# Kernel optimization log

Measured on AMD Instinct MI355X. Metric: run time of the kernel, lower is better.

Reference implementation:

```python
import jax, jax.numpy as jnp
import numpy as np

B = 1024
FEAT_C = [64, 64, 128, 256, 512]    # channel dim of each intermediate feature map
SPATIAL = [1024, 1024, 256, 64, 16]  # flattened HxW of each map (32x32 input)
STRIDES = [1, 1, 2, 4, 8]
NUM_CLASS = 10


def _conv(x, w, b, s):
    y = jax.lax.conv_general_dilated(x, w, (s, s), 'SAME',
                                     dimension_numbers=('NCHW', 'OIHW', 'NCHW'))
    return y + b[None, :, None, None]


def setup_inputs() -> dict:
    key = jax.random.key(0)
    ks = iter(jax.random.split(key, 64))
    nrm = lambda shape, scale=1.0: jax.random.normal(next(ks), shape, jnp.float32) * scale
    inp = {'x': nrm((B, 3, 32, 32))}
    inp['noise_w'] = nrm((15, 3, 3, 3), 0.1)
    inp['noise_b'] = nrm((15,), 0.01)
    for i, (c, s) in enumerate(zip(FEAT_C, SPATIAL)):
        inp[f'feat_w{i}'] = nrm((c, 3, 3, 3), 0.2)
        inp[f'feat_b{i}'] = nrm((c,), 0.01)
        inp[f'mu_w{i}'] = nrm((NUM_CLASS, s), 1.0 / np.sqrt(s))
        inp[f'mu_b{i}'] = nrm((NUM_CLASS,), 0.01)
        inp[f'std_w{i}'] = nrm((NUM_CLASS, s), 1.0 / np.sqrt(s))
        inp[f'std_b{i}'] = nrm((NUM_CLASS,), 0.01)
    inp['clf_w'] = nrm((1, 5), 0.5)
    inp['clf_b'] = nrm((1,), 0.01)
    return inp


def _forward(x, noise_w, noise_b, feat_ws, feat_bs, mu_ws, mu_bs, std_ws, std_bs, clf_w, clf_b):
    Bsz = x.shape[0]
    # noised_img = x.repeat([1,5,1,1]) + noise_layer(x)   -> [B,15,32,32]
    noised = jnp.tile(x, (1, 5, 1, 1)) + _conv(x, noise_w, noise_b, 1)
    ekey = jax.random.key(42)
    scores, means, stds = [], [], []
    for i in range(5):
        xi = noised[:, 3 * i:3 * (i + 1)]
        # stand-in for pretrained_model.intermediate_forward -> [B, C_i, S_i]
        f = _conv(xi, feat_ws[i], feat_bs[i], STRIDES[i]).reshape(Bsz, FEAT_C[i], -1)
        # Linear over flattened-spatial dim then transpose(1,2): [B, 10, C_i]
        x_mean = jnp.einsum('bcs,ks->bkc', f, mu_ws[i]) + mu_bs[i][None, :, None]
        x_std = jnp.einsum('bcs,ks->bkc', f, std_ws[i]) + std_bs[i][None, :, None]
        # original builds dense diag(std)^2 [B,10,C,C]; diagonal exploited analytically
        var = x_std * x_std                       # diag entries of x_variance (== scale_tril)
        eps = jax.random.normal(jax.random.fold_in(ekey, i), x_mean.shape, x_mean.dtype)
        d = var * eps                             # sample - mean = scale_tril @ eps (diagonal)
        # -0.5 * d^T inv(diag(var)) d, inverse done analytically instead of torch.inverse
        mahal = -0.5 * jnp.sum(d * d / var, axis=-1)   # [B, 10]
        idx = jnp.argmax(mahal, axis=1)
        scores.append(jnp.max(mahal, axis=1))
        means.append(jnp.take_along_axis(x_mean, idx[:, None, None], axis=1)[:, 0, :])
        stds.append(jnp.take_along_axis(x_std, idx[:, None, None], axis=1)[:, 0, :])
    score_stack = jnp.stack(scores, axis=1)       # [B, 5]
    out = (score_stack @ clf_w.T + clf_b)[:, 0]   # classifier Linear(5,1), squeeze(-1)
    return out, means, stds


def reference(x, noise_w, noise_b,
              feat_w0, feat_b0, mu_w0, mu_b0, std_w0, std_b0,
              feat_w1, feat_b1, mu_w1, mu_b1, std_w1, std_b1,
              feat_w2, feat_b2, mu_w2, mu_b2, std_w2, std_b2,
              feat_w3, feat_b3, mu_w3, mu_b3, std_w3, std_b3,
              feat_w4, feat_b4, mu_w4, mu_b4, std_w4, std_b4,
              clf_w, clf_b):
    feat_ws = [feat_w0, feat_w1, feat_w2, feat_w3, feat_w4]
    feat_bs = [feat_b0, feat_b1, feat_b2, feat_b3, feat_b4]
    mu_ws = [mu_w0, mu_w1, mu_w2, mu_w3, mu_w4]
    mu_bs = [mu_b0, mu_b1, mu_b2, mu_b3, mu_b4]
    std_ws = [std_w0, std_w1, std_w2, std_w3, std_w4]
    std_bs = [std_b0, std_b1, std_b2, std_b3, std_b4]
    out, means, stds = _forward(x, noise_w, noise_b, feat_ws, feat_bs,
                                mu_ws, mu_bs, std_ws, std_bs, clf_w, clf_b)
    return (out, *means, *stds)
```

## Files before the change

### kernel.cpp

```cpp
#include <hip/hip_runtime.h>
#include <cstdint>

#define B_SZ 1024

__host__ __device__ inline void tf2x32(uint32_t k0, uint32_t k1,
                                       uint32_t x0, uint32_t x1,
                                       uint32_t& o0, uint32_t& o1) {
  uint32_t ks2 = 0x1BD11BDAu ^ k0 ^ k1;
#define TF_RND(r) { x0 += x1; x1 = (x1 << (r)) | (x1 >> (32 - (r))); x1 ^= x0; }
  x0 += k0; x1 += k1;
  TF_RND(13) TF_RND(15) TF_RND(26) TF_RND(6)
  x0 += k1; x1 += ks2 + 1u;
  TF_RND(17) TF_RND(29) TF_RND(16) TF_RND(24)
  x0 += ks2; x1 += k0 + 2u;
  TF_RND(13) TF_RND(15) TF_RND(26) TF_RND(6)
  x0 += k0; x1 += k1 + 3u;
  TF_RND(17) TF_RND(29) TF_RND(16) TF_RND(24)
  x0 += k1; x1 += ks2 + 4u;
  TF_RND(13) TF_RND(15) TF_RND(26) TF_RND(6)
  x0 += ks2; x1 += k0 + 5u;
#undef TF_RND
  o0 = x0; o1 = x1;
}

__device__ inline float erfinv_f32(float x) {
  float w = -log1pf(-x * x);
  float p;
  if (w < 5.0f) {
    w -= 2.5f;
    p = 2.81022636e-08f;
    p = fmaf(p, w, 3.43273939e-07f);
    p = fmaf(p, w, -3.5233877e-06f);
    p = fmaf(p, w, -4.39150654e-06f);
    p = fmaf(p, w, 0.00021858087f);
    p = fmaf(p, w, -0.00125372503f);
    p = fmaf(p, w, -0.00417768164f);
    p = fmaf(p, w, 0.246640727f);
    p = fmaf(p, w, 1.50140941f);
  } else {
    w = sqrtf(w) - 3.0f;
    p = -0.000200214257f;
    p = fmaf(p, w, 0.000100950558f);
    p = fmaf(p, w, 0.00134934322f);
    p = fmaf(p, w, -0.00367342844f);
    p = fmaf(p, w, 0.00573950773f);
    p = fmaf(p, w, -0.0076224613f);
    p = fmaf(p, w, 0.00943887047f);
    p = fmaf(p, w, 1.00167406f);
    p = fmaf(p, w, 2.83297682f);
  }
  return p * x;
}

__device__ inline float jax_normal_pt(uint32_t k0, uint32_t k1, uint32_t e) {
  uint32_t o0, o1;
  tf2x32(k0, k1, 0u, e, o0, o1);
  uint32_t bits = o0 ^ o1;
  float f = __uint_as_float((bits >> 9) | 0x3f800000u) - 1.0f;
  const float LO = -0.99999994f;
  float u = fmaxf(LO, fmaf(f, 2.0f, LO));
  return 1.41421356f * erfinv_f32(u);
}

struct OodArgs {
  const float* x;
  const float* noise_w;
  const float* noise_b;
  const float* feat_w[5];
  const float* feat_b[5];
  const float* mu_w[5];
  const float* mu_b[5];
  const float* std_w[5];
  const float* std_b[5];
  float* mean_out[5];
  float* std_out[5];
  float* scores;
  float* gws;
  uint32_t fk0[5], fk1[5];
};

#define PITCH 35
#define CHSZ  (34 * PITCH)
#define XSZ   (3 * CHSZ)

#define A_XP   0
#define A_XI   3570
#define A_NW   7140
#define A_NB   7221
#define A_SMEM 7224

template<int S, int STRIDE>
__device__ __forceinline__ void stageA(const OodArgs& A_, float* smem, int i) {
  constexpr int Wd = 32 / STRIDE;

  const int b = blockIdx.x;
  const int t = threadIdx.x;

  float* s_xp = smem + A_XP;
  float* s_xi = smem + A_XI;
  float* s_nw = smem + A_NW;
  float* s_nb = smem + A_NB;

  for (int p = t; p < 2 * XSZ; p += 320) smem[p] = 0.0f;
  if (t < 81) s_nw[t] = A_.noise_w[81 * i + t];
  if (t < 3)  s_nb[t] = A_.noise_b[3 * i + t];
  __syncthreads();
  const float* xb = A_.x + (size_t)b * 3072;
  for (int p = t; p < 3072; p += 320) {
    int ci = p >> 10; int rr = p & 1023; int yy = rr >> 5; int xx = rr & 31;
    s_xp[ci * CHSZ + (yy + 1) * PITCH + (xx + 1)] = xb[p];
  }
  __syncthreads();

  #pragma unroll
  for (int co = 0; co < 3; ++co) {
    float nwr[27];
    #pragma unroll
    for (int j = 0; j < 27; ++j) nwr[j] = s_nw[co * 27 + j];
    const float nb = s_nb[co];
    for (int p = t; p < 1024; p += 320) {
      const int base = (p >> 5) * PITCH + (p & 31);
      float a = nb;
      #pragma unroll
      for (int c2 = 0; c2 < 3; ++c2) {
        #pragma unroll
        for (int q = 0; q < 9; ++q)
          a = fmaf(s_xp[c2 * CHSZ + base + (q / 3) * PITCH + (q % 3)],
                   nwr[c2 * 9 + q], a);
      }
      s_xi[co * CHSZ + base + PITCH + 1] = a + s_xp[co * CHSZ + base + PITCH + 1];
    }
  }
  __syncthreads();

  const int G  = t >> 4;
  const int ss = t & 15;
  const int wh = G & 1;
  const int kk = G >> 1;
  const float* wsrc = (wh ? A_.std_w[i] : A_.mu_w[i]) + kk * S;
  float* gdst = A_.gws + (size_t)(b * 5 + i) * 560;

  if constexpr (STRIDE == 1) {
    const float* wr = wsrc + (2 * ss) * 32;
    const int rbase0 = (2 * ss) * PITCH;
    #pragma unroll
    for (int ci = 0; ci < 3; ++ci) {
      const int rb = ci * CHSZ + rbase0;
      float acc[10];
      #pragma unroll
      for (int j = 0; j < 10; ++j) acc[j] = 0.0f;
      float Av[4], Bv[4], Cv[4];
      #pragma unroll
      for (int u = 0; u < 4; ++u) {
        Av[u] = s_xi[rb + u * PITCH + 0];
        Bv[u] = s_xi[rb + u * PITCH + 1];
      }

#define WCOMP(V, L) ((L) == 0 ? (V).x : (L) == 1 ? (V).y : (L) == 2 ? (V).z : (V).w)
#define STEP(X, P, Q, R, W0, W1) { \
    _Pragma("unroll") \
    for (int u = 0; u < 4; ++u) R[u] = s_xi[rb + u * PITCH + (X) + 2]; \
    const float w0c = WCOMP(W0, (X) & 3); \
    const float w1c = WCOMP(W1, (X) & 3); \
    _Pragma("unroll") \
    for (int dy = 0; dy < 3; ++dy) { \
      acc[dy*3+0] = fmaf(w0c, P[dy], fmaf(w1c, P[dy+1], acc[dy*3+0])); \
      acc[dy*3+1] = fmaf(w0c, Q[dy], fmaf(w1c, Q[dy+1], acc[dy*3+1])); \
      acc[dy*3+2] = fmaf(w0c, R[dy], fmaf(w1c, R[dy+1], acc[dy*3+2])); \
    } \
    if (ci == 0) acc[9] += w0c + w1c; \
  }
#define G4_0(c) { const float4 w0 = *(const float4*)(wr + (c)); \
                  const float4 w1 = *(const float4*)(wr + 32 + (c)); \
    STEP((c)+0, Av, Bv, Cv, w0, w1) STEP((c)+1, Bv, Cv, Av, w0, w1) \
    STEP((c)+2, Cv, Av, Bv, w0, w1) STEP((c)+3, Av, Bv, Cv, w0, w1) }
#define G4_1(c) { const float4 w0 = *(const float4*)(wr + (c)); \
                  const float4 w1 = *(const float4*)(wr + 32 + (c)); \
    STEP((c)+0, Bv, Cv, Av, w0, w1) STEP((c)+1, Cv, Av, Bv, w0, w1) \
    STEP((c)+2, Av, Bv, Cv, w0, w1) STEP((c)+3, Bv, Cv, Av, w0, w1) }
#define G4_2(c) { const float4 w0 = *(const float4*)(wr + (c)); \
                  const float4 w1 = *(const float4*)(wr + 32 + (c)); \
    STEP((c)+0, Cv, Av, Bv, w0, w1) STEP((c)+1, Av, Bv, Cv, w0, w1) \
    STEP((c)+2, Bv, Cv, Av, w0, w1) STEP((c)+3, Cv, Av, Bv, w0, w1) }

      G4_0(0) G4_1(4) G4_2(8) G4_0(12) G4_1(16) G4_2(20) G4_0(24) G4_1(28)

#undef G4_0
#undef G4_1
#undef G4_2
#undef STEP
#undef WCOMP
      #pragma unroll
      for (int j = 0; j < 10; ++j) {
        float v = acc[j];
        v += __shfl_xor(v, 1, 64);
        v += __shfl_xor(v, 2, 64);
        v += __shfl_xor(v, 4, 64);
        v += __shfl_xor(v, 8, 64);
        acc[j] = v;
      }
      if (ss == 0) {
        #pragma unroll
        for (int j = 0; j < 9; ++j)
          gdst[(wh * 10 + kk) * 27 + ci * 9 + j] = acc[j];
        if (ci == 0) gdst[540 + wh * 10 + kk] = acc[9];
      }
    }
  } else {
    constexpr int PER = S / 16;
    #pragma unroll
    for (int ci = 0; ci < 3; ++ci) {
      float acc[10];
      #pragma unroll
      for (int j = 0; j < 10; ++j) acc[j] = 0.0f;
      #pragma unroll
      for (int u = 0; u < PER; ++u) {
        const int s  = ss * PER + u;
        const int yo = s / Wd, xo = s % Wd;
        const float wx = wsrc[s];
        #pragma unroll
        for (int dy = 0; dy < 3; ++dy) {
          const int base = ci * CHSZ + (yo * STRIDE + dy + 1) * PITCH + (xo * STRIDE + 1);
          #pragma unroll
          for (int dx = 0; dx < 3; ++dx)
            acc[dy * 3 + dx] = fmaf(wx, s_xi[base + dx], acc[dy * 3 + dx]);
        }
        if (ci == 0) acc[9] += wx;
      }
      #pragma unroll
      for (int j = 0; j < 10; ++j) {
        float v = acc[j];
        v += __shfl_xor(v, 1, 64);
        v += __shfl_xor(v, 2, 64);
        v += __shfl_xor(v, 4, 64);
        v += __shfl_xor(v, 8, 64);
        acc[j] = v;
      }
      if (ss == 0) {
        #pragma unroll
        for (int j = 0; j < 9; ++j)
          gdst[(wh * 10 + kk) * 27 + ci * 9 + j] = acc[j];
        if (ci == 0) gdst[540 + wh * 10 + kk] = acc[9];
      }
    }
  }
}

__global__ __launch_bounds__(320, 8)
void ood_a(OodArgs A_) {
  __shared__ float smem[A_SMEM];
  const int y = blockIdx.y;
  switch (y) {
    case 0:
    case 1: stageA<1024, 1>(A_, smem, y); break;
    case 2: stageA< 256, 2>(A_, smem, 2); break;
    case 3: stageA<  64, 4>(A_, smem, 3); break;
    default: stageA< 16, 8>(A_, smem, 4); break;
  }
}

template<int I, int C>
__device__ __forceinline__ void stageB(const OodArgs& A_, float* smem) {
  const int b = blockIdx.x;
  const int t = threadIdx.x;

  float* s_g   = smem;
  float* s_rs  = smem + 540;
  float* s_std = smem + 560;
  float* s_pt  = smem + 560 + 10 * C;
  int*   s_idx = (int*)(smem + 570 + 10 * C);

  const float* feat_w = A_.feat_w[I];
  const float* feat_b = A_.feat_b[I];
  const uint32_t fk0 = A_.fk0[I], fk1 = A_.fk1[I];

  const float* gsrc = A_.gws + (size_t)(b * 5 + I) * 560;
  for (int p = t; p < 560; p += 320) smem[p] = gsrc[p];
  __syncthreads();

  for (int v = t; v < 10 * C; v += 320) {
    const int k2 = v / C; const int c = v - k2 * C;
    const float* fw = feat_w + c * 27;
    float a2 = 0.0f;
    #pragma unroll
    for (int j = 0; j < 27; ++j) a2 = fmaf(s_g[(10 + k2) * 27 + j], fw[j], a2);
    a2 = fmaf(feat_b[c], s_rs[10 + k2], a2) + A_.std_b[I][k2];
    s_std[v] = a2;
  }
  __syncthreads();

  {
    const int g  = t >> 6;
    const int ln = t & 63;
    float m0 = 0.0f, m1 = 0.0f;
    for (int c = ln; c < C; c += 64) {
      {
        const float sd  = s_std[g * C + c];
        const float eps = jax_normal_pt(fk0, fk1, (uint32_t)((b * 10 + g) * C + c));
        m0 = fmaf(sd * sd, eps * eps, m0);
      }
      {
        const float sd  = s_std[(g + 5) * C + c];
        const float eps = jax_normal_pt(fk0, fk1, (uint32_t)((b * 10 + g + 5) * C + c));
        m1 = fmaf(sd * sd, eps * eps, m1);
      }
    }
    #pragma unroll
    for (int off = 32; off > 0; off >>= 1) {
      m0 += __shfl_down(m0, off, 64);
      m1 += __shfl_down(m1, off, 64);
    }
    if (ln == 0) { s_pt[g] = m0; s_pt[g + 5] = m1; }
  }
  __syncthreads();
  if (t == 0) {
    float best = -INFINITY; int bi = 0;
    #pragma unroll
    for (int k2 = 0; k2 < 10; ++k2) {
      float m = -0.5f * s_pt[k2];
      if (m > best) { best = m; bi = k2; }
    }
    A_.scores[b * 5 + I] = best;
    *s_idx = bi;
  }
  __syncthreads();

  const int idx = *s_idx;
  for (int c = t; c < C; c += 320) {
    const float* fw = feat_w + c * 27;
    float a1 = 0.0f;
    #pragma unroll
    for (int j = 0; j < 27; ++j) a1 = fmaf(s_g[idx * 27 + j], fw[j], a1);
    a1 = fmaf(feat_b[c], s_rs[idx], a1) + A_.mu_b[I][idx];
    A_.mean_out[I][(size_t)b * C + c] = a1;
    A_.std_out[I][(size_t)b * C + c]  = s_std[idx * C + c];
  }
}

__global__ __launch_bounds__(320)
void ood_b(OodArgs A_) {
  __shared__ float smem[571 + 5120];
  switch (blockIdx.y) {
    case 0: stageB<0,  64>(A_, smem); break;
    case 1: stageB<1,  64>(A_, smem); break;
    case 2: stageB<2, 128>(A_, smem); break;
    case 3: stageB<3, 256>(A_, smem); break;
    default: stageB<4, 512>(A_, smem); break;
  }
}

__global__ void ood_clf(const float* __restrict__ scores,
                        const float* __restrict__ clf_w,
                        const float* __restrict__ clf_b,
                        float* __restrict__ out) {
  int b = blockIdx.x * blockDim.x + threadIdx.x;
  if (b < B_SZ) {
    float acc = clf_b[0];
    #pragma unroll
    for (int i = 0; i < 5; ++i) acc = fmaf(scores[b * 5 + i], clf_w[i], acc);
    out[b] = acc;
  }
}

extern "C" void kernel_launch(void* const* d_in, const int* in_sizes, int n_in,
                              void* d_out, int out_size, void* d_ws, size_t ws_size,
                              hipStream_t stream) {
  (void)in_sizes; (void)n_in; (void)out_size; (void)ws_size;
  const float* clf_w = (const float*)d_in[33];
  const float* clf_b = (const float*)d_in[34];
  float* out = (float*)d_out;
  float* ws  = (float*)d_ws;

  OodArgs A_;
  A_.x       = (const float*)d_in[0];
  A_.noise_w = (const float*)d_in[1];
  A_.noise_b = (const float*)d_in[2];
  const size_t NMEAN = 1048576;
  const size_t moff[5] = {1024, 66560, 132096, 263168, 525312};
  for (int i = 0; i < 5; ++i) {
    A_.feat_w[i]   = (const float*)d_in[3 + 6 * i];
    A_.feat_b[i]   = (const float*)d_in[4 + 6 * i];
    A_.mu_w[i]     = (const float*)d_in[5 + 6 * i];
    A_.mu_b[i]     = (const float*)d_in[6 + 6 * i];
    A_.std_w[i]    = (const float*)d_in[7 + 6 * i];
    A_.std_b[i]    = (const float*)d_in[8 + 6 * i];
    A_.mean_out[i] = out + moff[i];
    A_.std_out[i]  = out + moff[i] + NMEAN;
    tf2x32(0u, 42u, 0u, (uint32_t)i, A_.fk0[i], A_.fk1[i]);
  }
  A_.scores = ws;
  A_.gws    = ws + 5120;

  ood_a<<<dim3(B_SZ, 5), 320, 0, stream>>>(A_);
  ood_b<<<dim3(B_SZ, 5), 320, 0, stream>>>(A_);
  ood_clf<<<(B_SZ + 255) / 256, 256, 0, stream>>>(A_.scores, clf_w, clf_b, out);
}
```

Baseline: 322.4 us.

## Remap stage A reduction so each thread computes two output classes per spatial row

```diff
diff --git a/kernel.cpp b/kernel.cpp
--- a/kernel.cpp
+++ b/kernel.cpp
@@ -92,7 +92,6 @@
 template<int S, int STRIDE>
 __device__ __forceinline__ void stageA(const OodArgs& A_, float* smem, int i) {
   constexpr int Wd = 32 / STRIDE;
-
   const int b = blockIdx.x;
   const int t = threadIdx.x;
 
@@ -107,7 +106,7 @@
   __syncthreads();
   const float* xb = A_.x + (size_t)b * 3072;
   for (int p = t; p < 3072; p += 320) {
-    int ci = p >> 10; int rr = p & 1023; int yy = rr >> 5; int xx = rr & 31;
+    int ci = p >> 10, rr = p & 1023, yy = rr >> 5, xx = rr & 31;
     s_xp[ci * CHSZ + (yy + 1) * PITCH + (xx + 1)] = xb[p];
   }
   __syncthreads();
@@ -133,53 +132,82 @@
   }
   __syncthreads();
 
-  const int G  = t >> 4;
-  const int ss = t & 15;
-  const int wh = G & 1;
-  const int kk = G >> 1;
-  const float* wsrc = (wh ? A_.std_w[i] : A_.mu_w[i]) + kk * S;
+  const int g  = t >> 5;
+  const int ss = t & 31;
+  const int wh = g & 1;
+  const int k0 = (g >> 1) * 2;
+  const float* wbase = (wh ? A_.std_w[i] : A_.mu_w[i]) + k0 * S;
   float* gdst = A_.gws + (size_t)(b * 5 + i) * 560;
 
+#define REDUCE_WRITE(ci_) { \
+    _Pragma("unroll") \
+    for (int j = 0; j < 9; ++j) { \
+      float v0 = a0[j], v1 = a1[j]; \
+      v0 += __shfl_xor(v0, 1, 64);  v1 += __shfl_xor(v1, 1, 64); \
+      v0 += __shfl_xor(v0, 2, 64);  v1 += __shfl_xor(v1, 2, 64); \
+      v0 += __shfl_xor(v0, 4, 64);  v1 += __shfl_xor(v1, 4, 64); \
+      v0 += __shfl_xor(v0, 8, 64);  v1 += __shfl_xor(v1, 8, 64); \
+      v0 += __shfl_xor(v0, 16, 64); v1 += __shfl_xor(v1, 16, 64); \
+      a0[j] = v0; a1[j] = v1; \
+    } \
+    if ((ci_) == 0) { \
+      rs0 += __shfl_xor(rs0, 1, 64); rs0 += __shfl_xor(rs0, 2, 64); \
+      rs0 += __shfl_xor(rs0, 4, 64); rs0 += __shfl_xor(rs0, 8, 64); \
+      rs0 += __shfl_xor(rs0, 16, 64); \
+      rs1 += __shfl_xor(rs1, 1, 64); rs1 += __shfl_xor(rs1, 2, 64); \
+      rs1 += __shfl_xor(rs1, 4, 64); rs1 += __shfl_xor(rs1, 8, 64); \
+      rs1 += __shfl_xor(rs1, 16, 64); \
+    } \
+    if (ss == 0) { \
+      _Pragma("unroll") \
+      for (int j = 0; j < 9; ++j) { \
+        gdst[(wh * 10 + k0) * 27 + (ci_) * 9 + j]     = a0[j]; \
+        gdst[(wh * 10 + k0 + 1) * 27 + (ci_) * 9 + j] = a1[j]; \
+      } \
+      if ((ci_) == 0) { \
+        gdst[540 + wh * 10 + k0]     = rs0; \
+        gdst[540 + wh * 10 + k0 + 1] = rs1; \
+      } \
+    } }
+
   if constexpr (STRIDE == 1) {
-    const float* wr = wsrc + (2 * ss) * 32;
-    const int rbase0 = (2 * ss) * PITCH;
+    const float* wr = wbase + ss * 32;
     #pragma unroll
     for (int ci = 0; ci < 3; ++ci) {
-      const int rb = ci * CHSZ + rbase0;
-      float acc[10];
+      const int rb = ci * CHSZ + ss * PITCH;
+      float a0[9], a1[9];
       #pragma unroll
-      for (int j = 0; j < 10; ++j) acc[j] = 0.0f;
-      float Av[4], Bv[4], Cv[4];
+      for (int j = 0; j < 9; ++j) { a0[j] = 0.0f; a1[j] = 0.0f; }
+      float rs0 = 0.0f, rs1 = 0.0f;
+      float Av[3], Bv[3], Cv[3];
       #pragma unroll
-      for (int u = 0; u < 4; ++u) {
-        Av[u] = s_xi[rb + u * PITCH + 0];
+      for (int u = 0; u < 3; ++u) {
+        Av[u] = s_xi[rb + u * PITCH];
         Bv[u] = s_xi[rb + u * PITCH + 1];
       }
-
 #define WCOMP(V, L) ((L) == 0 ? (V).x : (L) == 1 ? (V).y : (L) == 2 ? (V).z : (V).w)
-#define STEP(X, P, Q, R, W0, W1) { \
+#define STEP(X, P_, Q_, R_, W0, W1) { \
     _Pragma("unroll") \
-    for (int u = 0; u < 4; ++u) R[u] = s_xi[rb + u * PITCH + (X) + 2]; \
+    for (int u = 0; u < 3; ++u) R_[u] = s_xi[rb + u * PITCH + (X) + 2]; \
     const float w0c = WCOMP(W0, (X) & 3); \
     const float w1c = WCOMP(W1, (X) & 3); \
     _Pragma("unroll") \
     for (int dy = 0; dy < 3; ++dy) { \
-      acc[dy*3+0] = fmaf(w0c, P[dy], fmaf(w1c, P[dy+1], acc[dy*3+0])); \
-      acc[dy*3+1] = fmaf(w0c, Q[dy], fmaf(w1c, Q[dy+1], acc[dy*3+1])); \
-      acc[dy*3+2] = fmaf(w0c, R[dy], fmaf(w1c, R[dy+1], acc[dy*3+2])); \
+      a0[dy*3+0] = fmaf(w0c, P_[dy], a0[dy*3+0]); a1[dy*3+0] = fmaf(w1c, P_[dy], a1[dy*3+0]); \
+      a0[dy*3+1] = fmaf(w0c, Q_[dy], a0[dy*3+1]); a1[dy*3+1] = fmaf(w1c, Q_[dy], a1[dy*3+1]); \
+      a0[dy*3+2] = fmaf(w0c, R_[dy], a0[dy*3+2]); a1[dy*3+2] = fmaf(w1c, R_[dy], a1[dy*3+2]); \
     } \
-    if (ci == 0) acc[9] += w0c + w1c; \
-  }
+    if (ci == 0) { rs0 += w0c; rs1 += w1c; } }
 #define G4_0(c) { const float4 w0 = *(const float4*)(wr + (c)); \
-                  const float4 w1 = *(const float4*)(wr + 32 + (c)); \
+                  const float4 w1 = *(const float4*)(wr + S + (c)); \
     STEP((c)+0, Av, Bv, Cv, w0, w1) STEP((c)+1, Bv, Cv, Av, w0, w1) \
     STEP((c)+2, Cv, Av, Bv, w0, w1) STEP((c)+3, Av, Bv, Cv, w0, w1) }
 #define G4_1(c) { const float4 w0 = *(const float4*)(wr + (c)); \
-                  const float4 w1 = *(const float4*)(wr + 32 + (c)); \
+                  const float4 w1 = *(const float4*)(wr + S + (c)); \
     STEP((c)+0, Bv, Cv, Av, w0, w1) STEP((c)+1, Cv, Av, Bv, w0, w1) \
     STEP((c)+2, Av, Bv, Cv, w0, w1) STEP((c)+3, Bv, Cv, Av, w0, w1) }
 #define G4_2(c) { const float4 w0 = *(const float4*)(wr + (c)); \
-                  const float4 w1 = *(const float4*)(wr + 32 + (c)); \
+                  const float4 w1 = *(const float4*)(wr + S + (c)); \
     STEP((c)+0, Cv, Av, Bv, w0, w1) STEP((c)+1, Av, Bv, Cv, w0, w1) \
     STEP((c)+2, Bv, Cv, Av, w0, w1) STEP((c)+3, Cv, Av, Bv, w0, w1) }
 
@@ -190,63 +218,43 @@
 #undef G4_2
 #undef STEP
 #undef WCOMP
+      REDUCE_WRITE(ci)
+    }
+  } else {
+    constexpr int PER = (S >= 32) ? (S / 32) : 1;
+    #pragma unroll
+    for (int ci = 0; ci < 3; ++ci) {
+      float a0[9], a1[9];
       #pragma unroll
-      for (int j = 0; j < 10; ++j) {
-        float v = acc[j];
-        v += __shfl_xor(v, 1, 64);
-        v += __shfl_xor(v, 2, 64);
-        v += __shfl_xor(v, 4, 64);
-        v += __shfl_xor(v, 8, 64);
-        acc[j] = v;
+      for (int j = 0; j < 9; ++j) { a0[j] = 0.0f; a1[j] = 0.0f; }
+      float rs0 = 0.0f, rs1 = 0.0f;
+      if (S >= 32 || ss < S) {
+        #pragma unroll
+        for (int u = 0; u < PER; ++u) {
+          const int s  = (S >= 32) ? (ss * PER + u) : ss;
+          const int yo = s / Wd, xo = s % Wd;
+          const float wx0 = wbase[s];
+          const float wx1 = wbase[S + s];
+          #pragma unroll
+          for (int dy = 0; dy < 3; ++dy) {
+            const int ba = ci * CHSZ + (yo * STRIDE + dy + 1) * PITCH + (xo * STRIDE + 1);
+            #pragma unroll
+            for (int dx = 0; dx < 3; ++dx) {
+              const float v = s_xi[ba + dx];
+              a0[dy*3+dx] = fmaf(wx0, v, a0[dy*3+dx]);
+              a1[dy*3+dx] = fmaf(wx1, v, a1[dy*3+dx]);
+            }
+          }
+          if (ci == 0) { rs0 += wx0; rs1 += wx1; }
+        }
       }
-      if (ss == 0) {
-        #pragma unroll
-        for (int j = 0; j < 9; ++j)
-          gdst[(wh * 10 + kk) * 27 + ci * 9 + j] = acc[j];
-        if (ci == 0) gdst[540 + wh * 10 + kk] = acc[9];
-      }
-    }
-  } else {
-    constexpr int PER = S / 16;
-    #pragma unroll
-    for (int ci = 0; ci < 3; ++ci) {
-      float acc[10];
-      #pragma unroll
-      for (int j = 0; j < 10; ++j) acc[j] = 0.0f;
-      #pragma unroll
-      for (int u = 0; u < PER; ++u) {
-        const int s  = ss * PER + u;
-        const int yo = s / Wd, xo = s % Wd;
-        const float wx = wsrc[s];
-        #pragma unroll
-        for (int dy = 0; dy < 3; ++dy) {
-          const int base = ci * CHSZ + (yo * STRIDE + dy + 1) * PITCH + (xo * STRIDE + 1);
-          #pragma unroll
-          for (int dx = 0; dx < 3; ++dx)
-            acc[dy * 3 + dx] = fmaf(wx, s_xi[base + dx], acc[dy * 3 + dx]);
-        }
-        if (ci == 0) acc[9] += wx;
-      }
-      #pragma unroll
-      for (int j = 0; j < 10; ++j) {
-        float v = acc[j];
-        v += __shfl_xor(v, 1, 64);
-        v += __shfl_xor(v, 2, 64);
-        v += __shfl_xor(v, 4, 64);
-        v += __shfl_xor(v, 8, 64);
-        acc[j] = v;
-      }
-      if (ss == 0) {
-        #pragma unroll
-        for (int j = 0; j < 9; ++j)
-          gdst[(wh * 10 + kk) * 27 + ci * 9 + j] = acc[j];
-        if (ci == 0) gdst[540 + wh * 10 + kk] = acc[9];
-      }
-    }
-  }
-}
-
-__global__ __launch_bounds__(320, 8)
+      REDUCE_WRITE(ci)
+    }
+  }
+#undef REDUCE_WRITE
+}
+
+__global__ __launch_bounds__(320)
 void ood_a(OodArgs A_) {
   __shared__ float smem[A_SMEM];
   const int y = blockIdx.y;
```

New measurement: 358.2 us. 11.1% more time.
